# Performance work log

Hardware: AMD Instinct MI355X
Metric: run time of the kernel (lower is better)

## Reference

```python
import math
import jax, jax.numpy as jnp
import numpy as np

BLOCK = 128
QMAX = 7.0            # 2**(4-1) - 1
ALPHA = 2.5139        # optimal Gaussian scale for 4 bits
N_LEVELS = 2 * 7 + 1  # 15
TRUST = ALPHA / N_LEVELS


def _build_hadamard(size: int) -> np.ndarray:
    H = np.ones((1, 1), dtype=np.float64)
    while H.shape[0] < size:
        H = np.block([[H, H], [H, -H]])
    return (H / math.sqrt(size)).astype(np.float32)


def _hadamard_rotate(x, H):
    # blockwise rotation along last dim; H is symmetric orthogonal so this is
    # its own inverse
    *batch, dim = x.shape
    bs = H.shape[0]
    return (x.reshape(*batch, dim // bs, bs) @ H).reshape(*batch, dim)


def setup_inputs() -> dict:
    key = jax.random.key(0)
    x = jax.random.normal(key, (4, 4096, 4096), dtype=jnp.float32)
    H = jnp.asarray(_build_hadamard(BLOCK))
    return {"x": x, "H": H}


def reference(x, H):
    x_h = _hadamard_rotate(x, H)
    # RMS over last dim
    std = jnp.maximum(jnp.sqrt(jnp.mean(x_h * x_h, axis=-1, keepdims=True)), 1e-8)
    step = (ALPHA * std) / QMAX
    xq = jnp.clip(jnp.round(x_h / step), -QMAX, QMAX) * step
    mask = (jnp.abs(xq - x_h) <= std * TRUST).astype(x_h.dtype)
    # straight-through: gradient flows only through x_h * mask
    out_h = x_h * mask + jax.lax.stop_gradient(xq - x_h * mask)
    return _hadamard_rotate(out_h, H)
```

## Files before the change

kernel.cpp:

```cpp
#include <hip/hip_runtime.h>


#define HTQ_ALPHA 2.5139f
#define HTQ_QMAX  7.0f

typedef float vfloat4 __attribute__((ext_vector_type(4)));

template <int CTRL>
__device__ __forceinline__ float dpp_perm(float f) {
    int r = __builtin_amdgcn_update_dpp(__float_as_int(f), __float_as_int(f),
                                        CTRL, 0xF, 0xF, true);
    return __int_as_float(r);
}

template <int MASK>
__device__ __forceinline__ float swz_xor(float f) {
    int r = __builtin_amdgcn_ds_swizzle(__float_as_int(f), (MASK << 10) | 0x1F);
    return __int_as_float(r);
}

#define CROSS_STAGE(GETP, BIT)                                   \
    {                                                            \
        const float sg = (lane & (BIT)) ? -1.0f : 1.0f;          \
        _Pragma("unroll")                                        \
        for (int i = 0; i < 64; ++i) {                           \
            float p = GETP(v[i]);                                \
            v[i] = fmaf(sg, v[i], p);                            \
        }                                                        \
    }

__device__ __forceinline__ void fwht128(float v[64], int lane) {
#pragma unroll
    for (int g = 0; g < 16; ++g) {
        float a0 = v[4 * g], a1 = v[4 * g + 1], a2 = v[4 * g + 2], a3 = v[4 * g + 3];
        float t0 = a0 + a1, t1 = a0 - a1, t2 = a2 + a3, t3 = a2 - a3;
        v[4 * g]     = t0 + t2;
        v[4 * g + 1] = t1 + t3;
        v[4 * g + 2] = t0 - t2;
        v[4 * g + 3] = t1 - t3;
    }
    CROSS_STAGE(dpp_perm<0xB1>, 1)
    CROSS_STAGE(dpp_perm<0x4E>, 2)
    CROSS_STAGE(swz_xor<4>, 4)
#pragma unroll
    for (int i = 0; i < 64; ++i) {
        if (i & 4) continue;
        float a = v[i], b = v[i + 4];
        v[i] = a + b;
        v[i + 4] = a - b;
    }
#pragma unroll
    for (int i = 0; i < 64; ++i) {
        if (i & 8) continue;
        float a = v[i], b = v[i + 8];
        v[i] = a + b;
        v[i + 8] = a - b;
    }
}

__global__ __launch_bounds__(256) void htq_kernel(const float* __restrict__ x,
                                                  float* __restrict__ out) {
    const int gid  = blockIdx.x * 256 + threadIdx.x;
    const int row  = gid >> 6;
    const int lane = threadIdx.x & 63;
    const int oct  = lane >> 3;
    const int sub  = lane & 7;

    const size_t base = (size_t)row * 4096 + (size_t)(oct * 128 + sub * 4);

    float v[64];
    vfloat4* v4 = reinterpret_cast<vfloat4*>(v);
    const vfloat4* g4 = reinterpret_cast<const vfloat4*>(x + base);
#pragma unroll
    for (int t = 0; t < 16; ++t)
        v4[t] = __builtin_nontemporal_load(&g4[(t >> 2) * 256 + (t & 3) * 8]);

    fwht128(v, lane);

    float ss = 0.0f;
#pragma unroll
    for (int i = 0; i < 64; ++i) ss = fmaf(v[i], v[i], ss);
#pragma unroll
    for (int m = 1; m < 64; m <<= 1) ss += __shfl_xor(ss, m, 64);

    float std_y = sqrtf(ss * (1.0f / 4096.0f));
    std_y = fmaxf(std_y, 1.1313708499e-7f);
    const float step  = (HTQ_ALPHA * std_y) / HTQ_QMAX;
    const float inv   = 1.0f / step;
    const float step2 = step * 0.0078125f;

#pragma unroll
    for (int i = 0; i < 64; ++i) {
        const float xv = v[i];
        float q0 = xv * inv;
        float rr = fmaf(-q0, step, xv);
        float q  = fmaf(rr, inv, q0);
        float r  = rintf(q);
        r = fminf(fmaxf(r, -HTQ_QMAX), HTQ_QMAX);
        v[i] = r * step2;
    }

    fwht128(v, lane);

    vfloat4* o4 = reinterpret_cast<vfloat4*>(out + base);
#pragma unroll
    for (int t = 0; t < 16; ++t)
        __builtin_nontemporal_store(v4[t], &o4[(t >> 2) * 256 + (t & 3) * 8]);
}

extern "C" void kernel_launch(void* const* d_in, const int* in_sizes, int n_in,
                              void* d_out, int out_size, void* d_ws, size_t ws_size,
                              hipStream_t stream) {
    const float* x = (const float*)d_in[0];
    float* out = (float*)d_out;

    const int n    = in_sizes[0];
    const int rows = n / 4096;
    const int blocks = (rows * 64) / 256;

    hipLaunchKernelGGL(htq_kernel, dim3(blocks), dim3(256), 0, stream, x, out);
}
```

Measured before the change: 428.0 us.

## Split each row across two wavefronts with 32 values per lane

Measured after the change: 426.7 us. Within noise of the previous version (-0.3%).

```diff
diff --git a/kernel.cpp b/kernel.cpp
--- a/kernel.cpp
+++ b/kernel.cpp
@@ -13,25 +13,19 @@
     return __int_as_float(r);
 }
 
-template <int MASK>
-__device__ __forceinline__ float swz_xor(float f) {
-    int r = __builtin_amdgcn_ds_swizzle(__float_as_int(f), (MASK << 10) | 0x1F);
-    return __int_as_float(r);
-}
-
 #define CROSS_STAGE(GETP, BIT)                                   \
     {                                                            \
         const float sg = (lane & (BIT)) ? -1.0f : 1.0f;          \
         _Pragma("unroll")                                        \
-        for (int i = 0; i < 64; ++i) {                           \
+        for (int i = 0; i < 32; ++i) {                           \
             float p = GETP(v[i]);                                \
             v[i] = fmaf(sg, v[i], p);                            \
         }                                                        \
     }
 
-__device__ __forceinline__ void fwht128(float v[64], int lane) {
+__device__ __forceinline__ void fwht128(float v[32], int lane) {
 #pragma unroll
-    for (int g = 0; g < 16; ++g) {
+    for (int g = 0; g < 8; ++g) {
         float a0 = v[4 * g], a1 = v[4 * g + 1], a2 = v[4 * g + 2], a3 = v[4 * g + 3];
         float t0 = a0 + a1, t1 = a0 - a1, t2 = a2 + a3, t3 = a2 - a3;
         v[4 * g]     = t0 + t2;
@@ -41,47 +35,61 @@
     }
     CROSS_STAGE(dpp_perm<0xB1>, 1)
     CROSS_STAGE(dpp_perm<0x4E>, 2)
-    CROSS_STAGE(swz_xor<4>, 4)
 #pragma unroll
-    for (int i = 0; i < 64; ++i) {
+    for (int i = 0; i < 32; ++i) {
         if (i & 4) continue;
         float a = v[i], b = v[i + 4];
         v[i] = a + b;
         v[i + 4] = a - b;
     }
 #pragma unroll
-    for (int i = 0; i < 64; ++i) {
+    for (int i = 0; i < 32; ++i) {
         if (i & 8) continue;
         float a = v[i], b = v[i + 8];
         v[i] = a + b;
         v[i + 8] = a - b;
     }
+#pragma unroll
+    for (int i = 0; i < 32; ++i) {
+        if (i & 16) continue;
+        float a = v[i], b = v[i + 16];
+        v[i] = a + b;
+        v[i + 16] = a - b;
+    }
 }
 
-__global__ __launch_bounds__(256) void htq_kernel(const float* __restrict__ x,
-                                                  float* __restrict__ out) {
-    const int gid  = blockIdx.x * 256 + threadIdx.x;
-    const int row  = gid >> 6;
+__global__ __launch_bounds__(256, 8) void htq_kernel(const float* __restrict__ x,
+                                                     float* __restrict__ out) {
+    const int wv   = threadIdx.x >> 6;
     const int lane = threadIdx.x & 63;
-    const int oct  = lane >> 3;
-    const int sub  = lane & 7;
+    const int gw   = blockIdx.x * 4 + wv;
+    const int row  = gw >> 1;
+    const int half = gw & 1;
+    const int blk  = lane >> 2;
+    const int sub  = lane & 3;
 
-    const size_t base = (size_t)row * 4096 + (size_t)(oct * 128 + sub * 4);
+    const size_t base = (size_t)row * 4096 + (size_t)half * 2048
+                      + (size_t)(blk * 128 + sub * 4);
 
-    float v[64];
+    float v[32];
     vfloat4* v4 = reinterpret_cast<vfloat4*>(v);
     const vfloat4* g4 = reinterpret_cast<const vfloat4*>(x + base);
 #pragma unroll
-    for (int t = 0; t < 16; ++t)
-        v4[t] = __builtin_nontemporal_load(&g4[(t >> 2) * 256 + (t & 3) * 8]);
+    for (int s = 0; s < 8; ++s)
+        v4[s] = __builtin_nontemporal_load(&g4[s * 4]);
 
     fwht128(v, lane);
 
     float ss = 0.0f;
 #pragma unroll
-    for (int i = 0; i < 64; ++i) ss = fmaf(v[i], v[i], ss);
+    for (int i = 0; i < 32; ++i) ss = fmaf(v[i], v[i], ss);
 #pragma unroll
     for (int m = 1; m < 64; m <<= 1) ss += __shfl_xor(ss, m, 64);
+
+    __shared__ float red[4];
+    if (lane == 0) red[wv] = ss;
+    __syncthreads();
+    ss = red[wv] + red[wv ^ 1];
 
     float std_y = sqrtf(ss * (1.0f / 4096.0f));
     std_y = fmaxf(std_y, 1.1313708499e-7f);
@@ -90,7 +98,7 @@
     const float step2 = step * 0.0078125f;
 
 #pragma unroll
-    for (int i = 0; i < 64; ++i) {
+    for (int i = 0; i < 32; ++i) {
         const float xv = v[i];
         float q0 = xv * inv;
         float rr = fmaf(-q0, step, xv);
@@ -104,8 +112,8 @@
 
     vfloat4* o4 = reinterpret_cast<vfloat4*>(out + base);
 #pragma unroll
-    for (int t = 0; t < 16; ++t)
-        __builtin_nontemporal_store(v4[t], &o4[(t >> 2) * 256 + (t & 3) * 8]);
+    for (int s = 0; s < 8; ++s)
+        __builtin_nontemporal_store(v4[s], &o4[s * 4]);
 }
 
 extern "C" void kernel_launch(void* const* d_in, const int* in_sizes, int n_in,
@@ -116,7 +124,7 @@
 
     const int n    = in_sizes[0];
     const int rows = n / 4096;
-    const int blocks = (rows * 64) / 256;
+    const int blocks = rows / 2;
 
     hipLaunchKernelGGL(htq_kernel, dim3(blocks), dim3(256), 0, stream, x, out);
 }
```
